# Kernel tuning notes

Hardware: AMD Instinct MI355X
Metric: run time of the kernel (lower is better)

The kernel has to match this reference:

```python
import jax, jax.numpy as jnp
import numpy as np

B, T_RED, C = 16, 512, 512
MAX_DUR = 16


def setup_inputs() -> dict:
    key = jax.random.key(0)
    rng = np.random.default_rng(0)
    durs = np.zeros((B, T_RED), dtype=np.int32)
    for b in range(B):
        nv = int(rng.integers(T_RED // 2, T_RED + 1))
        durs[b, :nv] = rng.integers(1, MAX_DUR + 1, size=nv)
    target_T = durs.sum(axis=1).astype(np.int32)
    pooled_x = jax.random.normal(key, (B, T_RED, C), dtype=jnp.float32)
    return {
        "pooled_x": pooled_x,
        "durations": jnp.asarray(durs),
        "target_T": jnp.asarray(target_T),
    }


def reference(pooled_x, durations, target_T):
    # pooled_x: [B, T_red, C]; durations: [B, T_red] int (0 = pad); target_T: [B]
    Bv, T_red, Cv = pooled_x.shape
    max_len = int(jnp.max(target_T))  # concrete (eager) like the torch .item()

    # torch: valid_durs = durations[b][durations[b] > 0]; feats = pooled_x[b, :num_valid]
    # -> stably compact nonzero durations to the front; pair with leading features.
    order = jnp.argsort(jnp.where(durations > 0, 0, 1), axis=1, stable=True)
    d = jnp.take_along_axis(durations, order, axis=1)            # [B, T_red]
    csum = jnp.cumsum(d, axis=1)                                 # [B, T_red]

    t = jnp.arange(max_len, dtype=csum.dtype)                    # [max_len]
    # repeat_interleave inverse: output frame t belongs to segment
    # s = searchsorted(csum, t, 'right')  (csum[s-1] <= t < csum[s])
    seg = jax.vmap(lambda c: jnp.searchsorted(c, t, side="right"))(csum)  # [B, max_len]
    seg = jnp.minimum(seg, T_red - 1)

    total = csum[:, -1]                                          # len(repeat_interleave result)
    curr_len = jnp.minimum(total, target_T)                      # [B]
    valid = t[None, :] < curr_len[:, None]                       # [B, max_len]

    gathered = jnp.take_along_axis(pooled_x, seg[:, :, None], axis=1)  # [B, max_len, C]
    x_restored = jnp.where(valid[:, :, None], gathered, jnp.zeros((), pooled_x.dtype))
    new_mask = jnp.where(valid, 0, 1).astype(jnp.int32)          # 0 = valid, 1 = padded
    return x_restored, new_mask
```

## Files before the change

kernel.cpp:

```cpp
#include <hip/hip_runtime.h>
#include <hip/hip_bf16.h>

#define B_DIM 16
#define T_RED 512
#define C_DIM 512

__global__ void build_rowmap(const int* __restrict__ durations,
                             int* __restrict__ rowsrc, int max_len) {
    const int b = blockIdx.x;
    const int tid = threadIdx.x;

    __shared__ int scan[T_RED];
    __shared__ int dcomp[T_RED];
    __shared__ int csum[T_RED];

    const int d = durations[b * T_RED + tid];
    const int f = (d > 0) ? 1 : 0;

    scan[tid] = f;
    __syncthreads();
    for (int off = 1; off < T_RED; off <<= 1) {
        int v = scan[tid];
        int add = (tid >= off) ? scan[tid - off] : 0;
        __syncthreads();
        scan[tid] = v + add;
        __syncthreads();
    }

    dcomp[tid] = 0;
    __syncthreads();
    if (f) dcomp[scan[tid] - 1] = d;
    __syncthreads();

    csum[tid] = dcomp[tid];
    __syncthreads();
    for (int off = 1; off < T_RED; off <<= 1) {
        int v = csum[tid];
        int add = (tid >= off) ? csum[tid - off] : 0;
        __syncthreads();
        csum[tid] = v + add;
        __syncthreads();
    }

    const int total = csum[T_RED - 1];
    const int myd   = dcomp[tid];
    const int start = csum[tid] - myd;

    for (int k = 0; k < myd; ++k)
        rowsrc[b * max_len + start + k] = tid;

    for (int t = total + tid; t < max_len; t += T_RED)
        rowsrc[b * max_len + t] = -1;
}

__global__ void scatter_rows(const float* __restrict__ x,
                             const int* __restrict__ rowsrc,
                             float* __restrict__ out_x,
                             float* __restrict__ out_mask,
                             int max_len) {
    const int t = blockIdx.x;
    const int b = blockIdx.y;
    const int c4 = threadIdx.x;

    const int src = rowsrc[b * max_len + t];

    float4 v = make_float4(0.f, 0.f, 0.f, 0.f);
    if (src >= 0) {
        v = ((const float4*)x)[(size_t)(b * T_RED + src) * (C_DIM / 4) + c4];
    }
    ((float4*)out_x)[((size_t)b * max_len + t) * (C_DIM / 4) + c4] = v;

    if (c4 == 0) {
        out_mask[(size_t)b * max_len + t] = (src >= 0) ? 0.0f : 1.0f;
    }
}

extern "C" void kernel_launch(void* const* d_in, const int* in_sizes, int n_in,
                              void* d_out, int out_size, void* d_ws, size_t ws_size,
                              hipStream_t stream) {
    const float* pooled_x  = (const float*)d_in[0];
    const int*   durations = (const int*)d_in[1];

    const int max_len = out_size / (B_DIM * (C_DIM + 1));

    float* out_x    = (float*)d_out;
    float* out_mask = out_x + (size_t)B_DIM * max_len * C_DIM;

    int* rowsrc = (int*)d_ws;

    build_rowmap<<<B_DIM, T_RED, 0, stream>>>(durations, rowsrc, max_len);

    dim3 grid(max_len, B_DIM);
    scatter_rows<<<grid, C_DIM / 4, 0, stream>>>(pooled_x, rowsrc, out_x, out_mask, max_len);
}
```

Baseline: 170.4 us.

## Use wave-shuffle block scans and process four rows per scatter block

The shared-memory Hillis-Steele scans in the row-map builder are replaced with a wave-level shuffle scan plus a small cross-wave scan, which cuts the number of block barriers. Row indices are stored as flattened global source rows, so the copy kernel treats output as a flat row list. Each copy block now has 256 threads and handles four rows, two per thread, which cuts block count and gives each thread two independent loads in flight. The main cost is the bandwidth-bound copy, so the gain is limited to lower launch and scheduling overhead.

```diff
diff --git a/kernel.cpp b/kernel.cpp
--- a/kernel.cpp
+++ b/kernel.cpp
@@ -5,73 +5,94 @@
 #define T_RED 512
 #define C_DIM 512
 
+__device__ inline int wave_incl_scan(int v) {
+    #pragma unroll
+    for (int off = 1; off < 64; off <<= 1) {
+        int n = __shfl_up(v, off, 64);
+        if ((threadIdx.x & 63) >= off) v += n;
+    }
+    return v;
+}
+
+__device__ inline int block_incl_scan(int v, int* wsum ) {
+    const int lane = threadIdx.x & 63;
+    const int wid  = threadIdx.x >> 6;
+    int s = wave_incl_scan(v);
+    if (lane == 63) wsum[wid] = s;
+    __syncthreads();
+    if (wid == 0 && lane < 8) {
+        int w = wsum[lane];
+        #pragma unroll
+        for (int off = 1; off < 8; off <<= 1) {
+            int n = __shfl_up(w, off, 8);
+            if (lane >= off) w += n;
+        }
+        wsum[lane] = w;
+    }
+    __syncthreads();
+    if (wid > 0) s += wsum[wid - 1];
+    return s;
+}
+
 __global__ void build_rowmap(const int* __restrict__ durations,
                              int* __restrict__ rowsrc, int max_len) {
     const int b = blockIdx.x;
     const int tid = threadIdx.x;
 
-    __shared__ int scan[T_RED];
+    __shared__ int wsum[8];
     __shared__ int dcomp[T_RED];
-    __shared__ int csum[T_RED];
+    __shared__ int csum_s[T_RED];
 
     const int d = durations[b * T_RED + tid];
     const int f = (d > 0) ? 1 : 0;
 
-    scan[tid] = f;
-    __syncthreads();
-    for (int off = 1; off < T_RED; off <<= 1) {
-        int v = scan[tid];
-        int add = (tid >= off) ? scan[tid - off] : 0;
-        __syncthreads();
-        scan[tid] = v + add;
-        __syncthreads();
-    }
-
+    const int pos = block_incl_scan(f, wsum);
     dcomp[tid] = 0;
     __syncthreads();
-    if (f) dcomp[scan[tid] - 1] = d;
+    if (f) dcomp[pos - 1] = d;
     __syncthreads();
 
-    csum[tid] = dcomp[tid];
+    const int myd = dcomp[tid];
     __syncthreads();
-    for (int off = 1; off < T_RED; off <<= 1) {
-        int v = csum[tid];
-        int add = (tid >= off) ? csum[tid - off] : 0;
-        __syncthreads();
-        csum[tid] = v + add;
-        __syncthreads();
-    }
+    const int cs = block_incl_scan(myd, wsum);
+    csum_s[tid] = cs;
+    __syncthreads();
 
-    const int total = csum[T_RED - 1];
-    const int myd   = dcomp[tid];
-    const int start = csum[tid] - myd;
+    const int total = csum_s[T_RED - 1];
+    const int start = cs - myd;
+    const int srcrow = b * T_RED + tid;
 
     for (int k = 0; k < myd; ++k)
-        rowsrc[b * max_len + start + k] = tid;
+        rowsrc[b * max_len + start + k] = srcrow;
 
     for (int t = total + tid; t < max_len; t += T_RED)
         rowsrc[b * max_len + t] = -1;
 }
 
-__global__ void scatter_rows(const float* __restrict__ x,
+__global__ void scatter_rows(const float4* __restrict__ x4,
                              const int* __restrict__ rowsrc,
-                             float* __restrict__ out_x,
+                             float4* __restrict__ out4,
                              float* __restrict__ out_mask,
-                             int max_len) {
-    const int t = blockIdx.x;
-    const int b = blockIdx.y;
-    const int c4 = threadIdx.x;
+                             int nrows) {
+    const int sub = threadIdx.x >> 7;
+    const int c4  = threadIdx.x & 127;
+    const int r0  = blockIdx.x * 4 + sub;
+    const int r1  = r0 + 2;
 
-    const int src = rowsrc[b * max_len + t];
+    const int s0 = (r0 < nrows) ? rowsrc[r0] : -1;
+    const int s1 = (r1 < nrows) ? rowsrc[r1] : -1;
 
-    float4 v = make_float4(0.f, 0.f, 0.f, 0.f);
-    if (src >= 0) {
-        v = ((const float4*)x)[(size_t)(b * T_RED + src) * (C_DIM / 4) + c4];
-    }
-    ((float4*)out_x)[((size_t)b * max_len + t) * (C_DIM / 4) + c4] = v;
+    float4 v0 = make_float4(0.f, 0.f, 0.f, 0.f);
+    float4 v1 = make_float4(0.f, 0.f, 0.f, 0.f);
+    if (s0 >= 0) v0 = x4[(size_t)s0 * (C_DIM / 4) + c4];
+    if (s1 >= 0) v1 = x4[(size_t)s1 * (C_DIM / 4) + c4];
+
+    if (r0 < nrows) out4[(size_t)r0 * (C_DIM / 4) + c4] = v0;
+    if (r1 < nrows) out4[(size_t)r1 * (C_DIM / 4) + c4] = v1;
 
     if (c4 == 0) {
-        out_mask[(size_t)b * max_len + t] = (src >= 0) ? 0.0f : 1.0f;
+        if (r0 < nrows) out_mask[r0] = (s0 >= 0) ? 0.0f : 1.0f;
+        if (r1 < nrows) out_mask[r1] = (s1 >= 0) ? 0.0f : 1.0f;
     }
 }
 
@@ -82,14 +103,15 @@
     const int*   durations = (const int*)d_in[1];
 
     const int max_len = out_size / (B_DIM * (C_DIM + 1));
+    const int nrows   = B_DIM * max_len;
 
     float* out_x    = (float*)d_out;
-    float* out_mask = out_x + (size_t)B_DIM * max_len * C_DIM;
+    float* out_mask = out_x + (size_t)nrows * C_DIM;
 
     int* rowsrc = (int*)d_ws;
 
     build_rowmap<<<B_DIM, T_RED, 0, stream>>>(durations, rowsrc, max_len);
 
-    dim3 grid(max_len, B_DIM);
-    scatter_rows<<<grid, C_DIM / 4, 0, stream>>>(pooled_x, rowsrc, out_x, out_mask, max_len);
+    scatter_rows<<<(nrows + 3) / 4, 256, 0, stream>>>(
+        (const float4*)pooled_x, rowsrc, (float4*)out_x, out_mask, nrows);
 }
```

Result: faster. 160.7 us (-5.7%).
